# Kernel tuning notes

Measured on AMD Instinct MI355X. Metric: run time of the kernel, lower is better.

Reference implementation:

```python
import jax, jax.numpy as jnp
import numpy as np

I, L, T, S = 128, 8, 128, 128   # input neurons, topo batches, neurons per batch, fan-in span
BIG = 1e9
EPS = 1e-5


def setup_inputs() -> dict:
    key = jax.random.key(0)
    ks = jax.random.split(key, 7)
    x = jax.random.normal(ks[0], (I,), jnp.float32)
    # per-neuron weights|bias, scaled down for numerical stability of softmax/gelu chain
    W = jax.random.normal(ks[1], (L, T, S + 1), jnp.float32) * 0.05
    mask = (jax.random.uniform(ks[2], (L, T, S)) > 0.5).astype(jnp.float32)  # DAG connectivity
    attn_t = jax.random.normal(ks[3], (L, 3, S, S + 1), jnp.float32) * 0.05      # topo q/k/v (weight|bias)
    attn_n = jax.random.normal(ks[4], (L, T, 3, S, S + 1), jnp.float32) * 0.05   # per-neuron q/k/v
    # additive attention mask: attend only over a neuron's actual inputs
    attn_mask_n = BIG * (1.0 - mask[:, :, :, None] * mask[:, :, None, :])        # (L,T,S,S)
    norm_params = jnp.stack([jnp.ones((L, S)), jnp.zeros((L, S))], 1) \
        + 0.1 * jax.random.normal(ks[5], (L, 2, S), jnp.float32)                 # gamma, beta
    ada = jnp.ones((L, T, 2), jnp.float32) \
        + 0.1 * jax.random.normal(ks[6], (L, T, 2), jnp.float32)                 # gain, amplification
    span_ids = jnp.arange(L * S, dtype=jnp.int32).reshape(L, S)    # gather indices per topo batch
    tb_ids = I + jnp.arange(L * T, dtype=jnp.int32).reshape(L, T)  # scatter indices per topo batch
    return dict(x=x, W=W, mask=mask, attn_t=attn_t, attn_n=attn_n,
                attn_mask_n=attn_mask_n, norm_params=norm_params, ada=ada,
                span_ids=span_ids, tb_ids=tb_ids)


def _attention(qkv, vals, amask):
    # qkv: (3, S, S+1) stacked query/key/value (weight|bias); vals: (S,)
    wq, bq = qkv[0, :, :-1], qkv[0, :, -1]
    wk, bk = qkv[1, :, :-1], qkv[1, :, -1]
    wv, bv = qkv[2, :, :-1], qkv[2, :, -1]
    q = wq @ vals + bq
    k = wk @ vals + bk
    v = wv @ vals + bv
    scores = jnp.outer(q, k) * jax.lax.rsqrt(jnp.float32(vals.shape[0])) - amask
    return jax.nn.softmax(scores) @ v + vals  # residual connection


def _forward(x, W, mask, attn_t, attn_n, attn_mask_n, norm_params, ada, span_ids, tb_ids):
    values = jnp.zeros((I + L * T,), x.dtype).at[jnp.arange(I)].set(x)
    for b in range(L):  # fixed, small topological batch order
        vals = values[span_ids[b]]                                  # gather fan-in span (S,)
        mu = jnp.mean(vals)
        var = jnp.var(vals)
        vals = (vals - mu) * jax.lax.rsqrt(var + EPS)               # topo norm (standardize)
        vals = vals * norm_params[b, 0] + norm_params[b, 1]
        vals = _attention(attn_t[b], vals, 0.0)                     # topo-level self-attention
        # neuron-level self-attention, vmapped over the batch's T neurons -> (T, S)
        vals_n = jax.vmap(_attention, in_axes=(0, None, 0))(attn_n[b], vals, attn_mask_n[b])
        w, bias = W[b, :, :-1], W[b, :, -1]
        aff = jnp.einsum('ts,ts->t', w * mask[b], vals_n) + bias    # masked affine per neuron
        if b == L - 1:
            out = aff                                               # output neurons: identity transform
        else:
            out = jax.nn.gelu(aff * ada[b, :, 0]) * ada[b, :, 1]    # adaptive activation a*sigma(b*x)
        values = values.at[tb_ids[b]].set(out)
    return values[tb_ids[L - 1]]


def reference(x, W, mask, attn_t, attn_n, attn_mask_n, norm_params, ada, span_ids, tb_ids):
    return _forward(x, W, mask, attn_t, attn_n, attn_mask_n, norm_params, ada, span_ids, tb_ids)
```

## Files before the change

kernel.cpp:

```cpp
#include <hip/hip_runtime.h>
#include <math.h>

#define L_DIM 8
#define T_DIM 128
#define S_DIM 128
#define SP1   129
#define SPAD  132
#define BIGF  1000000000.0f
#define EPSF  1e-5f
#define NTHREADS 1024
#define NWAVES 16
#define NCHUNKS 132

template<int CTRL>
__device__ __forceinline__ float dpp_add_part(float x) {
    int r = __builtin_amdgcn_update_dpp(0, __float_as_int(x), CTRL, 0xF, 0xF, false);
    return __int_as_float(r);
}
__device__ __forceinline__ float dpp16Sum15(float x) {
    x += dpp_add_part<0x111>(x);
    x += dpp_add_part<0x112>(x);
    x += dpp_add_part<0x114>(x);
    x += dpp_add_part<0x118>(x);
    return x;
}
__device__ __forceinline__ float dppSum63(float x) {
    x += dpp_add_part<0x111>(x);
    x += dpp_add_part<0x112>(x);
    x += dpp_add_part<0x114>(x);
    x += dpp_add_part<0x118>(x);
    x += dpp_add_part<0x142>(x);
    x += dpp_add_part<0x143>(x);
    return x;
}
__device__ __forceinline__ float lane63(float x) {
    return __int_as_float(__builtin_amdgcn_readlane(__float_as_int(x), 63));
}

__device__ __forceinline__ void wg_bar() {
    asm volatile("s_waitcnt lgkmcnt(0)" ::: "memory");
    __builtin_amdgcn_s_barrier();
    asm volatile("" ::: "memory");
}
__device__ __forceinline__ void wg_bar_vm() {
    asm volatile("s_waitcnt vmcnt(0) lgkmcnt(0)" ::: "memory");
    __builtin_amdgcn_s_barrier();
    asm volatile("" ::: "memory");
}

__device__ __forceinline__ void gld_lds16(const float* g, float* l) {
    __builtin_amdgcn_global_load_lds(
        (const __attribute__((address_space(1))) void*)g,
        (__attribute__((address_space(3))) void*)l,
        16, 0, 0);
}

__device__ __forceinline__ void stage_nqk(const float* __restrict__ src,
                                          float* __restrict__ lds,
                                          int wid, int lane) {
#pragma unroll
    for (int k = 0; k < 9; ++k) {
        int c = wid + k * NWAVES;
        if (c < NCHUNKS) {
            int s   = c * 64 + lane;
            int row = s / 33;
            int w   = s - row * 33;
            gld_lds16(src + (size_t)row * SP1 + w * 4, lds + c * 256);
        }
    }
}

__device__ __forceinline__ void mv_glb(const float* __restrict__ mat,
                                       const float in[8], int li, int r_base,
                                       float* __restrict__ dst) {
#pragma unroll
    for (int p = 0; p < 2; ++p) {
        int r = r_base + p * 4;
        const float* row = mat + (size_t)r * SP1;
        float acc = 0.0f;
#pragma unroll
        for (int e = 0; e < 8; ++e) acc = fmaf(row[li * 8 + e], in[e], acc);
        acc = dpp16Sum15(acc);
        if (li == 15) dst[r] = acc + row[128];
    }
}

__device__ __forceinline__ void mv_stage(const float* __restrict__ mat,
                                         const float in[8], int li, int r_base,
                                         float* __restrict__ dst) {
#pragma unroll
    for (int p = 0; p < 2; ++p) {
        int r = r_base + p * 4;
        const float* row = mat + r * SPAD;
        float acc = 0.0f;
#pragma unroll
        for (int e = 0; e < 8; ++e) acc = fmaf(row[li * 8 + e], in[e], acc);
        acc = dpp16Sum15(acc);
        if (li == 15) dst[r] = acc + row[128];
    }
}

__device__ __forceinline__ void mv_regs(const float wv[2][8], const float wb[2],
                                        const float in[8], int li, int r_base,
                                        float* __restrict__ dst) {
#pragma unroll
    for (int p = 0; p < 2; ++p) {
        float acc = 0.0f;
#pragma unroll
        for (int e = 0; e < 8; ++e) acc = fmaf(wv[p][e], in[e], acc);
        acc = dpp16Sum15(acc);
        if (li == 15) dst[r_base + p * 4] = acc + wb[p];
    }
}

__device__ __forceinline__ void row_prefetch(const float* __restrict__ mb_,
                                             int li, int r0, int r1,
                                             float arr[2][8], float* b0, float* b1) {
#pragma unroll
    for (int p = 0; p < 2; ++p) {
        int r = p ? r1 : r0;
        const float* row = mb_ + (size_t)r * SP1 + li * 8;
#pragma unroll
        for (int e = 0; e < 8; ++e) arr[p][e] = row[e];
        float bb = mb_[(size_t)r * SP1 + 128];
        if (p) *b1 = bb; else *b0 = bb;
    }
}

__device__ __forceinline__ void attn_sm_t(int li, int r_base,
                                          const float* __restrict__ lds_q,
                                          const float* __restrict__ lds_k,
                                          const float* __restrict__ lds_v,
                                          const float* __restrict__ resid,
                                          float* __restrict__ lds_out)
{
    const float scale = 0.08838834764831845f;
    float kx[8], vx[8];
#pragma unroll
    for (int e = 0; e < 8; ++e) { kx[e] = lds_k[li * 8 + e]; vx[e] = lds_v[li * 8 + e]; }
#pragma unroll
    for (int p = 0; p < 2; ++p) {
        int r = r_base + p * 4;
        float qs = lds_q[r] * scale;
        float den = 0.0f, num = 0.0f;
#pragma unroll
        for (int e = 0; e < 8; ++e) {
            float ee = __expf(qs * kx[e]);
            den += ee;
            num = fmaf(ee, vx[e], num);
        }
        den = dpp16Sum15(den);
        num = dpp16Sum15(num);
        if (li == 15) lds_out[r] = num / den + resid[r];
    }
}

__global__ __launch_bounds__(NTHREADS)
void net_kernel(const float* __restrict__ x,
                const float* __restrict__ W,
                const float* __restrict__ maskp,
                const float* __restrict__ attn_t,
                const float* __restrict__ attn_n,
                const float* __restrict__ norm_params,
                const float* __restrict__ ada,
                float* __restrict__ out,
                unsigned long long* __restrict__ mbox)
{
    const int t    = blockIdx.x;
    const int tid  = threadIdx.x;
    const int lane = tid & 63;
    const int wid  = tid >> 6;
    const int li   = lane & 15;
    const int g    = lane >> 4;
    const int r0   = wid * 8 + g;
    const int r1   = r0 + 4;

    __shared__ float lds_nqk[2 * S_DIM * SPAD];
    __shared__ float lds_vals[S_DIM];
    __shared__ float lds_q[S_DIM], lds_k[S_DIM], lds_v[S_DIM];
    __shared__ float lds_tv[S_DIM];
    __shared__ float lds_aff[NWAVES];

    float nv[2][8];
    float nvb0, nvb1;

    {
        const float* srcn = attn_n + (size_t)t * 3 * S_DIM * SP1;
        stage_nqk(srcn, lds_nqk, wid, lane);
        row_prefetch(srcn + 2 * S_DIM * SP1, li, r0, r1, nv, &nvb0, &nvb1);
    }

    for (int b = 0; b < L_DIM; ++b) {
        const float* mrow = maskp + (size_t)(b * T_DIM + t) * S_DIM;
        const float* wrow = W + (size_t)(b * T_DIM + t) * SP1;
        float m1mj[8];
#pragma unroll
        for (int e = 0; e < 8; ++e) m1mj[e] = 1.0f - mrow[li * 8 + e];
        float mr0 = mrow[r0], mr1 = mrow[r1];
        float wr0 = wrow[r0], wr1 = wrow[r1];
        float wb  = (wid == 0) ? wrow[128] : 0.0f;

        if (wid == 0) {
            float np00 = norm_params[(b * 2 + 0) * S_DIM + lane];
            float np10 = norm_params[(b * 2 + 0) * S_DIM + lane + 64];
            float np01 = norm_params[(b * 2 + 1) * S_DIM + lane];
            float np11 = norm_params[(b * 2 + 1) * S_DIM + lane + 64];
            float v0, v1;
            if (b == 0) {
                v0 = x[lane]; v1 = x[lane + 64];
            } else {
                float a00 = ada[((b - 1) * T_DIM + lane) * 2 + 0];
                float a01 = ada[((b - 1) * T_DIM + lane) * 2 + 1];
                float a10 = ada[((b - 1) * T_DIM + lane + 64) * 2 + 0];
                float a11 = ada[((b - 1) * T_DIM + lane + 64) * 2 + 1];
                const unsigned long long* mb_ = mbox + (size_t)(b - 1) * T_DIM;
                unsigned long long u0, u1;
                do {
                    u0 = __hip_atomic_load(&mb_[lane], __ATOMIC_RELAXED, __HIP_MEMORY_SCOPE_AGENT);
                    u1 = __hip_atomic_load(&mb_[lane + 64], __ATOMIC_RELAXED, __HIP_MEMORY_SCOPE_AGENT);
                } while ((unsigned int)(u0 >> 32) != (unsigned int)b ||
                         (unsigned int)(u1 >> 32) != (unsigned int)b);
                {
                    float z = __uint_as_float((unsigned int)u0) * a00;
                    float z3 = z * z * z;
                    v0 = 0.5f * z * (1.0f + tanhf(0.7978845608028654f * (z + 0.044715f * z3))) * a01;
                }
                {
                    float z = __uint_as_float((unsigned int)u1) * a10;
                    float z3 = z * z * z;
                    v1 = 0.5f * z * (1.0f + tanhf(0.7978845608028654f * (z + 0.044715f * z3))) * a11;
                }
            }
            float s  = dppSum63(v0 + v1);
            float mu = lane63(s) * (1.0f / 128.0f);
            float d0 = v0 - mu, d1 = v1 - mu;
            float s2 = dppSum63(fmaf(d0, d0, d1 * d1));
            float rstd = rsqrtf(lane63(s2) * (1.0f / 128.0f) + EPSF);
            lds_vals[lane]      = d0 * rstd * np00 + np01;
            lds_vals[lane + 64] = d1 * rstd * np10 + np11;
        }
        wg_bar();

        {
            float iv[8];
#pragma unroll
            for (int e = 0; e < 8; ++e) iv[e] = lds_vals[li * 8 + e];
            const float* bb = attn_t + (size_t)b * 3 * S_DIM * SP1;
            mv_glb(bb,                    iv, li, r0, lds_q);
            mv_glb(bb + 1 * S_DIM * SP1,  iv, li, r0, lds_k);
            mv_glb(bb + 2 * S_DIM * SP1,  iv, li, r0, lds_v);
        }
        wg_bar();

        attn_sm_t(li, r0, lds_q, lds_k, lds_v, lds_vals, lds_tv);
        wg_bar_vm();

        {
            float tvv[8];
#pragma unroll
            for (int e = 0; e < 8; ++e) tvv[e] = lds_tv[li * 8 + e];
            mv_stage(lds_nqk,                 tvv, li, r0, lds_q);
            mv_stage(lds_nqk + S_DIM * SPAD,  tvv, li, r0, lds_k);
            float bv[2] = { nvb0, nvb1 };
            mv_regs(nv, bv, tvv, li, r0, lds_v);
        }
        wg_bar();

        if (b < L_DIM - 1) {
            const float* srcn = attn_n + (size_t)((b + 1) * T_DIM + t) * 3 * S_DIM * SP1;
            stage_nqk(srcn, lds_nqk, wid, lane);
            row_prefetch(srcn + 2 * S_DIM * SP1, li, r0, r1, nv, &nvb0, &nvb1);
        }

        {
            const float scale = 0.08838834764831845f;
            float kx[8], vx[8];
#pragma unroll
            for (int e = 0; e < 8; ++e) { kx[e] = lds_k[li * 8 + e]; vx[e] = lds_v[li * 8 + e]; }
            float o0 = 0.0f, o1 = 0.0f;
#pragma unroll
            for (int p = 0; p < 2; ++p) {
                int r = r0 + p * 4;
                float qs = lds_q[r] * scale;
                float bp = BIGF * (p ? mr1 : mr0);
                float den = 0.0f, num = 0.0f;
#pragma unroll
                for (int e = 0; e < 8; ++e) {
                    float s_ = fmaf(-bp, m1mj[e], qs * kx[e]);
                    float ee = __expf(s_);
                    den += ee;
                    num = fmaf(ee, vx[e], num);
                }
                den = dpp16Sum15(den);
                num = dpp16Sum15(num);
                float o = num / den + lds_tv[r];
                if (p) o1 = o; else o0 = o;
            }
            float part = (li == 15) ? (wr0 * mr0 * o0 + wr1 * mr1 * o1) : 0.0f;
            part = dppSum63(part);
            if (lane == 63) lds_aff[wid] = part;
        }
        wg_bar();

        if (wid == 0) {
            float pa = (lane < NWAVES) ? lds_aff[lane] : 0.0f;
            pa = dppSum63(pa);
            if (lane == 63) {
                float aff = pa + wb;
                if (b == L_DIM - 1) {
                    out[t] = aff;
                } else {
                    unsigned long long u =
                        ((unsigned long long)(unsigned int)(b + 1) << 32) |
                        (unsigned long long)__float_as_uint(aff);
                    __hip_atomic_store(&mbox[(size_t)b * T_DIM + t], u,
                                       __ATOMIC_RELAXED, __HIP_MEMORY_SCOPE_AGENT);
                }
            }
        }
    }
}

extern "C" void kernel_launch(void* const* d_in, const int* in_sizes, int n_in,
                              void* d_out, int out_size, void* d_ws, size_t ws_size,
                              hipStream_t stream) {
    const float* x           = (const float*)d_in[0];
    const float* W           = (const float*)d_in[1];
    const float* maskp       = (const float*)d_in[2];
    const float* attn_t      = (const float*)d_in[3];
    const float* attn_n      = (const float*)d_in[4];
    const float* norm_params = (const float*)d_in[6];
    const float* ada         = (const float*)d_in[7];
    float* out = (float*)d_out;

    unsigned long long* mbox = (unsigned long long*)d_ws;

    hipMemsetAsync(d_ws, 0, (size_t)(L_DIM - 1) * T_DIM * sizeof(unsigned long long), stream);

    void* args[] = { (void*)&x, (void*)&W, (void*)&maskp, (void*)&attn_t, (void*)&attn_n,
                     (void*)&norm_params, (void*)&ada, (void*)&out, (void*)&mbox };
    hipLaunchCooperativeKernel((const void*)net_kernel, dim3(T_DIM), dim3(NTHREADS),
                               args, 0, stream);
}
```

Before: 417.8 us.

## Skip loading masked-out neuron q/k/v rows and specialize waves for staging

Attention rows for masked-out inputs are no longer fetched. Their q/k/v weights come from the mask: v rows are zeroed and q/k rows are not staged into LDS, with the q score forced to zero. Staging moves from wide 16-byte chunks to 4-byte global-to-LDS loads issued only by waves 8-15, while waves 0-7 do the topo matvecs with four rows each. Mask and W loads move later in the loop. The aim is to cut global memory traffic roughly in half given the random mask, and to overlap staging with compute on separate waves. The cost is more, smaller load instructions and an uneven load across waves.

Result: slower. 466.6 us (+11.7%).

```diff
diff --git a/kernel.cpp b/kernel.cpp
--- a/kernel.cpp
+++ b/kernel.cpp
@@ -5,12 +5,11 @@
 #define T_DIM 128
 #define S_DIM 128
 #define SP1   129
-#define SPAD  132
+#define NSTRIDE 132
 #define BIGF  1000000000.0f
 #define EPSF  1e-5f
 #define NTHREADS 1024
 #define NWAVES 16
-#define NCHUNKS 132
 
 template<int CTRL>
 __device__ __forceinline__ float dpp_add_part(float x) {
@@ -42,40 +41,20 @@
     __builtin_amdgcn_s_barrier();
     asm volatile("" ::: "memory");
 }
-__device__ __forceinline__ void wg_bar_vm() {
-    asm volatile("s_waitcnt vmcnt(0) lgkmcnt(0)" ::: "memory");
-    __builtin_amdgcn_s_barrier();
-    asm volatile("" ::: "memory");
-}
-
-__device__ __forceinline__ void gld_lds16(const float* g, float* l) {
+
+__device__ __forceinline__ void gld_lds4(const float* g, float* l) {
     __builtin_amdgcn_global_load_lds(
         (const __attribute__((address_space(1))) void*)g,
         (__attribute__((address_space(3))) void*)l,
-        16, 0, 0);
-}
-
-__device__ __forceinline__ void stage_nqk(const float* __restrict__ src,
-                                          float* __restrict__ lds,
-                                          int wid, int lane) {
-#pragma unroll
-    for (int k = 0; k < 9; ++k) {
-        int c = wid + k * NWAVES;
-        if (c < NCHUNKS) {
-            int s   = c * 64 + lane;
-            int row = s / 33;
-            int w   = s - row * 33;
-            gld_lds16(src + (size_t)row * SP1 + w * 4, lds + c * 256);
-        }
-    }
-}
-
-__device__ __forceinline__ void mv_glb(const float* __restrict__ mat,
-                                       const float in[8], int li, int r_base,
-                                       float* __restrict__ dst) {
-#pragma unroll
-    for (int p = 0; p < 2; ++p) {
-        int r = r_base + p * 4;
+        4, 0, 0);
+}
+
+__device__ __forceinline__ void mv_glb4(const float* __restrict__ mat,
+                                        const float in[8], int li, int rb,
+                                        float* __restrict__ dst) {
+#pragma unroll
+    for (int p = 0; p < 4; ++p) {
+        int r = rb + 4 * p;
         const float* row = mat + (size_t)r * SP1;
         float acc = 0.0f;
 #pragma unroll
@@ -85,18 +64,19 @@
     }
 }
 
-__device__ __forceinline__ void mv_stage(const float* __restrict__ mat,
-                                         const float in[8], int li, int r_base,
-                                         float* __restrict__ dst) {
+__device__ __forceinline__ void mv_stage2(const float* __restrict__ mat,
+                                          const float* __restrict__ biasArr,
+                                          const float in[8], int li, int r_base,
+                                          float* __restrict__ dst) {
 #pragma unroll
     for (int p = 0; p < 2; ++p) {
         int r = r_base + p * 4;
-        const float* row = mat + r * SPAD;
+        const float* row = mat + r * NSTRIDE;
         float acc = 0.0f;
 #pragma unroll
         for (int e = 0; e < 8; ++e) acc = fmaf(row[li * 8 + e], in[e], acc);
         acc = dpp16Sum15(acc);
-        if (li == 15) dst[r] = acc + row[128];
+        if (li == 15) dst[r] = acc + biasArr[r];
     }
 }
 
@@ -110,20 +90,6 @@
         for (int e = 0; e < 8; ++e) acc = fmaf(wv[p][e], in[e], acc);
         acc = dpp16Sum15(acc);
         if (li == 15) dst[r_base + p * 4] = acc + wb[p];
-    }
-}
-
-__device__ __forceinline__ void row_prefetch(const float* __restrict__ mb_,
-                                             int li, int r0, int r1,
-                                             float arr[2][8], float* b0, float* b1) {
-#pragma unroll
-    for (int p = 0; p < 2; ++p) {
-        int r = p ? r1 : r0;
-        const float* row = mb_ + (size_t)r * SP1 + li * 8;
-#pragma unroll
-        for (int e = 0; e < 8; ++e) arr[p][e] = row[e];
-        float bb = mb_[(size_t)r * SP1 + 128];
-        if (p) *b1 = bb; else *b0 = bb;
     }
 }
 
@@ -175,7 +141,9 @@
     const int r0   = wid * 8 + g;
     const int r1   = r0 + 4;
 
-    __shared__ float lds_nqk[2 * S_DIM * SPAD];
+    __shared__ float lds_nq[S_DIM * NSTRIDE];
+    __shared__ float lds_nk[S_DIM * NSTRIDE];
+    __shared__ float lds_nqb[S_DIM], lds_nkb[S_DIM];
     __shared__ float lds_vals[S_DIM];
     __shared__ float lds_q[S_DIM], lds_k[S_DIM], lds_v[S_DIM];
     __shared__ float lds_tv[S_DIM];
@@ -186,20 +154,32 @@
 
     {
         const float* srcn = attn_n + (size_t)t * 3 * S_DIM * SP1;
-        stage_nqk(srcn, lds_nqk, wid, lane);
-        row_prefetch(srcn + 2 * S_DIM * SP1, li, r0, r1, nv, &nvb0, &nvb1);
+        if (wid >= 8) {
+            if (wid == 8)  gld_lds4(srcn + (size_t)lane * SP1 + 128, lds_nqb);
+            if (wid == 9)  gld_lds4(srcn + (size_t)(64 + lane) * SP1 + 128, lds_nqb + 64);
+            if (wid == 10) gld_lds4(srcn + (size_t)(S_DIM + lane) * SP1 + 128, lds_nkb);
+            if (wid == 11) gld_lds4(srcn + (size_t)(S_DIM + 64 + lane) * SP1 + 128, lds_nkb + 64);
+            const float* kb_ = srcn + S_DIM * SP1;
+#pragma unroll
+            for (int k2 = 0; k2 < 16; ++k2) {
+                int r = (wid - 8) + 8 * k2;
+                gld_lds4(srcn + (size_t)r * SP1 + lane,      lds_nq + r * NSTRIDE);
+                gld_lds4(srcn + (size_t)r * SP1 + 64 + lane, lds_nq + r * NSTRIDE + 64);
+                gld_lds4(kb_  + (size_t)r * SP1 + lane,      lds_nk + r * NSTRIDE);
+                gld_lds4(kb_  + (size_t)r * SP1 + 64 + lane, lds_nk + r * NSTRIDE + 64);
+            }
+        }
+        const float* vb_ = srcn + 2 * S_DIM * SP1;
+#pragma unroll
+        for (int e = 0; e < 8; ++e) {
+            nv[0][e] = vb_[(size_t)r0 * SP1 + li * 8 + e];
+            nv[1][e] = vb_[(size_t)r1 * SP1 + li * 8 + e];
+        }
+        nvb0 = vb_[(size_t)r0 * SP1 + 128];
+        nvb1 = vb_[(size_t)r1 * SP1 + 128];
     }
 
     for (int b = 0; b < L_DIM; ++b) {
-        const float* mrow = maskp + (size_t)(b * T_DIM + t) * S_DIM;
-        const float* wrow = W + (size_t)(b * T_DIM + t) * SP1;
-        float m1mj[8];
-#pragma unroll
-        for (int e = 0; e < 8; ++e) m1mj[e] = 1.0f - mrow[li * 8 + e];
-        float mr0 = mrow[r0], mr1 = mrow[r1];
-        float wr0 = wrow[r0], wr1 = wrow[r1];
-        float wb  = (wid == 0) ? wrow[128] : 0.0f;
-
         if (wid == 0) {
             float np00 = norm_params[(b * 2 + 0) * S_DIM + lane];
             float np10 = norm_params[(b * 2 + 0) * S_DIM + lane + 64];
@@ -241,26 +221,37 @@
         }
         wg_bar();
 
-        {
+        if (wid < 8) {
             float iv[8];
 #pragma unroll
             for (int e = 0; e < 8; ++e) iv[e] = lds_vals[li * 8 + e];
             const float* bb = attn_t + (size_t)b * 3 * S_DIM * SP1;
-            mv_glb(bb,                    iv, li, r0, lds_q);
-            mv_glb(bb + 1 * S_DIM * SP1,  iv, li, r0, lds_k);
-            mv_glb(bb + 2 * S_DIM * SP1,  iv, li, r0, lds_v);
+            int rb = wid * 16 + g;
+            mv_glb4(bb,                   iv, li, rb, lds_q);
+            mv_glb4(bb + 1 * S_DIM * SP1, iv, li, rb, lds_k);
+            mv_glb4(bb + 2 * S_DIM * SP1, iv, li, rb, lds_v);
         }
         wg_bar();
 
         attn_sm_t(li, r0, lds_q, lds_k, lds_v, lds_vals, lds_tv);
-        wg_bar_vm();
+        if (wid >= 8) asm volatile("s_waitcnt vmcnt(0)" ::: "memory");
+        wg_bar();
+
+        const float* mrow = maskp + (size_t)(b * T_DIM + t) * S_DIM;
+        const float* wrow = W + (size_t)(b * T_DIM + t) * SP1;
+        float m1mj[8];
+#pragma unroll
+        for (int e = 0; e < 8; ++e) m1mj[e] = 1.0f - mrow[li * 8 + e];
+        float mr0 = mrow[r0], mr1 = mrow[r1];
+        float wr0 = wrow[r0], wr1 = wrow[r1];
+        float wb  = (wid == 0) ? wrow[128] : 0.0f;
 
         {
             float tvv[8];
 #pragma unroll
             for (int e = 0; e < 8; ++e) tvv[e] = lds_tv[li * 8 + e];
-            mv_stage(lds_nqk,                 tvv, li, r0, lds_q);
-            mv_stage(lds_nqk + S_DIM * SPAD,  tvv, li, r0, lds_k);
+            mv_stage2(lds_nq, lds_nqb, tvv, li, r0, lds_q);
+            mv_stage2(lds_nk, lds_nkb, tvv, li, r0, lds_k);
             float bv[2] = { nvb0, nvb1 };
             mv_regs(nv, bv, tvv, li, r0, lds_v);
         }
@@ -268,8 +259,47 @@
 
         if (b < L_DIM - 1) {
             const float* srcn = attn_n + (size_t)((b + 1) * T_DIM + t) * 3 * S_DIM * SP1;
-            stage_nqk(srcn, lds_nqk, wid, lane);
-            row_prefetch(srcn + 2 * S_DIM * SP1, li, r0, r1, nv, &nvb0, &nvb1);
+            const float* mnx  = maskp + (size_t)((b + 1) * T_DIM + t) * S_DIM;
+            float mr0n = mnx[r0], mr1n = mnx[r1];
+            float mml = (wid >= 8 && lane < 16) ? mnx[(wid - 8) + 8 * lane] : 0.0f;
+            unsigned long long bal = __ballot(mml != 0.0f);
+            bool a0 = (mr0n != 0.0f), a1 = (mr1n != 0.0f);
+            const float* vb_ = srcn + 2 * S_DIM * SP1;
+            if (a0) {
+#pragma unroll
+                for (int e = 0; e < 8; ++e) nv[0][e] = vb_[(size_t)r0 * SP1 + li * 8 + e];
+                nvb0 = vb_[(size_t)r0 * SP1 + 128];
+            } else {
+#pragma unroll
+                for (int e = 0; e < 8; ++e) nv[0][e] = 0.0f;
+                nvb0 = 0.0f;
+            }
+            if (a1) {
+#pragma unroll
+                for (int e = 0; e < 8; ++e) nv[1][e] = vb_[(size_t)r1 * SP1 + li * 8 + e];
+                nvb1 = vb_[(size_t)r1 * SP1 + 128];
+            } else {
+#pragma unroll
+                for (int e = 0; e < 8; ++e) nv[1][e] = 0.0f;
+                nvb1 = 0.0f;
+            }
+            if (wid >= 8) {
+                if (wid == 8)  gld_lds4(srcn + (size_t)lane * SP1 + 128, lds_nqb);
+                if (wid == 9)  gld_lds4(srcn + (size_t)(64 + lane) * SP1 + 128, lds_nqb + 64);
+                if (wid == 10) gld_lds4(srcn + (size_t)(S_DIM + lane) * SP1 + 128, lds_nkb);
+                if (wid == 11) gld_lds4(srcn + (size_t)(S_DIM + 64 + lane) * SP1 + 128, lds_nkb + 64);
+                const float* kb_ = srcn + S_DIM * SP1;
+#pragma unroll
+                for (int k2 = 0; k2 < 16; ++k2) {
+                    if ((bal >> k2) & 1ull) {
+                        int r = (wid - 8) + 8 * k2;
+                        gld_lds4(srcn + (size_t)r * SP1 + lane,      lds_nq + r * NSTRIDE);
+                        gld_lds4(srcn + (size_t)r * SP1 + 64 + lane, lds_nq + r * NSTRIDE + 64);
+                        gld_lds4(kb_  + (size_t)r * SP1 + lane,      lds_nk + r * NSTRIDE);
+                        gld_lds4(kb_  + (size_t)r * SP1 + 64 + lane, lds_nk + r * NSTRIDE + 64);
+                    }
+                }
+            }
         }
 
         {
@@ -281,8 +311,10 @@
 #pragma unroll
             for (int p = 0; p < 2; ++p) {
                 int r = r0 + p * 4;
-                float qs = lds_q[r] * scale;
-                float bp = BIGF * (p ? mr1 : mr0);
+                float mrp = p ? mr1 : mr0;
+                float qv = lds_q[r];
+                float qs = (mrp == 0.0f) ? 0.0f : qv * scale;
+                float bp = BIGF * mrp;
                 float den = 0.0f, num = 0.0f;
 #pragma unroll
                 for (int e = 0; e < 8; ++e) {
```
